# Kernel optimization log

Hardware: AMD Instinct MI355X
Metric: run time of the kernel (lower is better)

Reference implementation:

```python
import jax, jax.numpy as jnp
import numpy as np

NUM_SELECTS = 2
NOISE_EPS = 0.01
LOSS_COEF = 0.01
INV_SQRT2 = 0.7071067811865476


def _phi(z):
    # standard normal CDF
    return 0.5 * (1.0 + jax.lax.erf(z * INV_SQRT2))


def _cv_squared(v, eps=1e-10):
    # torch .var() uses unbiased estimator (ddof=1)
    return jnp.var(v, ddof=1) / (jnp.mean(v) ** 2 + eps)


def setup_inputs() -> dict:
    key = jax.random.key(0)
    ks = jax.random.split(key, 5)
    T, D, E = 8192, 4096, 16
    return {
        "x": jax.random.normal(ks[0], (T, D), jnp.float32),
        "gate_w1": jax.random.normal(ks[1], (E, D), jnp.float32) * 0.02,
        "gate_w2": jax.random.normal(ks[2], (E, E), jnp.float32) * 0.02,
        "noise_w": jax.random.normal(ks[3], (E, D), jnp.float32) * 0.02,
        "noise": jax.random.normal(ks[4], (T, E), jnp.float32),
    }


def reference(x, gate_w1, gate_w2, noise_w, noise):
    T = x.shape[0]
    # gate network: Linear -> tanh -> Linear (no biases)
    logits_gate = jnp.tanh(x @ gate_w1.T) @ gate_w2.T          # [T, E]
    noise_control = jax.nn.softplus(x @ noise_w.T) + NOISE_EPS  # [T, E]
    logits_noise = noise * noise_control                        # [T, E]
    logits = logits_gate + logits_noise

    # top (k+1) for load-balancing thresholds
    top_logits, top_indices = jax.lax.top_k(logits, NUM_SELECTS + 1)
    top_k_logits = top_logits[:, :NUM_SELECTS]
    top_k_indices = top_indices[:, :NUM_SELECTS]
    top_k_scores = jax.nn.softmax(top_k_logits, axis=1)

    # importance: scatter top-k scores back to [T, E]
    rows = jnp.arange(T)[:, None]
    scores_filtered = jnp.zeros_like(logits).at[rows, top_k_indices].set(top_k_scores)
    importance = scores_filtered.sum(0)  # [E]

    # load: prob each expert would be in the top-k under the noise model
    thr_in = top_logits[:, NUM_SELECTS][:, None]        # (k+1)-th largest
    thr_out = top_logits[:, NUM_SELECTS - 1][:, None]   # k-th largest
    is_in = logits_noise > thr_in
    prob_if_in = _phi((logits_gate - thr_in) / noise_control)
    prob_if_out = _phi((logits_gate - thr_out) / noise_control)
    load = jnp.where(is_in, prob_if_in, prob_if_out).sum(0)  # [E]

    gate_loss = (_cv_squared(importance) + _cv_squared(load)) * LOSS_COEF
    return top_k_indices, top_k_scores, gate_loss
```

## Files before the change

kernel.cpp:

```cpp
#include <hip/hip_runtime.h>
#include <math.h>

#define TT 8192
#define DD 4096

typedef float  f32x4  __attribute__((ext_vector_type(4)));
typedef short  bf16x8 __attribute__((ext_vector_type(8)));
typedef unsigned int u32;

__global__ __launch_bounds__(128)
void split_w(const float* __restrict__ gw1, const float* __restrict__ nw,
             u32* __restrict__ wfrag) {
  const int s = blockIdx.x;
  const int t = threadIdx.x;
  const int h = t >> 6, l = t & 63;
  const int e = h * 16 + (l & 15);
  const float* src = ((e < 16) ? (gw1 + (size_t)e * DD) : (nw + (size_t)(e - 16) * DD))
                     + s * 32 + ((l >> 4) << 3);
  float f[8];
  *(float4*)&f[0] = *(const float4*)src;
  *(float4*)&f[4] = *(const float4*)(src + 4);
  u32 u0[8], u1[8], u2[8];
#pragma unroll
  for (int i = 0; i < 8; ++i) {
    u0[i] = __float_as_uint(f[i]);
    const float r1 = f[i] - __uint_as_float(u0[i] & 0xFFFF0000u);
    u1[i] = __float_as_uint(r1);
    const float r2 = r1 - __uint_as_float(u1[i] & 0xFFFF0000u);
    u2[i] = __float_as_uint(r2);
  }
  const size_t base = ((size_t)s * 2 + h) * 256 + l * 4;
#define PK(U) make_uint4((U[0]>>16)|(U[1]&0xFFFF0000u), (U[2]>>16)|(U[3]&0xFFFF0000u), \
                         (U[4]>>16)|(U[5]&0xFFFF0000u), (U[6]>>16)|(U[7]&0xFFFF0000u))
  *(uint4*)(wfrag + base)                 = PK(u0);
  *(uint4*)(wfrag + base + 128 * 512)     = PK(u1);
  *(uint4*)(wfrag + base + 2 * 128 * 512) = PK(u2);
#undef PK
}

__global__ __launch_bounds__(512, 4)
void gate_mega(const float* __restrict__ x, const u32* __restrict__ wfrag,
               const float* __restrict__ noise, const float* __restrict__ gw2,
               float* __restrict__ out, float* __restrict__ part2) {
  __shared__ float red[8][1024];
  __shared__ float sg2[256];
  const int t = threadIdx.x;
  const int w = t >> 6, l = t & 63;
  const int bid = blockIdx.x;
  const int rt = (bid & 7) * 32 + (bid >> 3);
  if (t < 256) sg2[t] = gw2[t];

  const int r = l & 15, c = l >> 4;
  const float* xp0 = x + (size_t)(rt * 32 + r) * DD + w * 512 + (c << 3);
  const float* xp1 = xp0 + (size_t)16 * DD;
  const u32* wfl = wfrag + (size_t)l * 4 + (size_t)(w * 16) * 512;

  f32x4 g00 = {0,0,0,0}, g01 = g00, g02 = g00, n00 = g00, n01 = g00, n02 = g00;
  f32x4 g10 = g00, g11 = g00, g12 = g00, n10 = g00, n11 = g00, n12 = g00;

#define SPLIT8(FP, A0, A1, A2) \
  u32 pk_[12] __attribute__((aligned(16))); \
  { _Pragma("unroll") for (int p = 0; p < 4; ++p) { \
      const float fa = FP[2*p], fb = FP[2*p+1]; \
      const u32  a  = __float_as_uint(fa); \
      const float ra1 = fa - __uint_as_float(a & 0xFFFF0000u); \
      const u32  a1 = __float_as_uint(ra1); \
      const float ra2 = ra1 - __uint_as_float(a1 & 0xFFFF0000u); \
      const u32  a2 = __float_as_uint(ra2); \
      const u32  b  = __float_as_uint(fb); \
      const float rb1 = fb - __uint_as_float(b & 0xFFFF0000u); \
      const u32  b1 = __float_as_uint(rb1); \
      const float rb2 = rb1 - __uint_as_float(b1 & 0xFFFF0000u); \
      const u32  b2 = __float_as_uint(rb2); \
      pk_[p]     = (a  >> 16) | (b  & 0xFFFF0000u); \
      pk_[4 + p] = (a1 >> 16) | (b1 & 0xFFFF0000u); \
      pk_[8 + p] = (a2 >> 16) | (b2 & 0xFFFF0000u); } } \
  const bf16x8 A0 = *(const bf16x8*)&pk_[0]; \
  const bf16x8 A1 = *(const bf16x8*)&pk_[4]; \
  const bf16x8 A2 = *(const bf16x8*)&pk_[8];

#pragma unroll 2
  for (int sl = 0; sl < 16; ++sl) {
    const u32* wb = wfl + (size_t)sl * 512;
    const bf16x8 bg0 = *(const bf16x8*)(wb);
    const bf16x8 bn0 = *(const bf16x8*)(wb + 256);
    const bf16x8 bg1 = *(const bf16x8*)(wb + 128 * 512);
    const bf16x8 bn1 = *(const bf16x8*)(wb + 128 * 512 + 256);
    const bf16x8 bg2 = *(const bf16x8*)(wb + 2 * 128 * 512);
    const bf16x8 bn2 = *(const bf16x8*)(wb + 2 * 128 * 512 + 256);

    {
      float f[8];
      *(float4*)&f[0] = *(const float4*)(xp0 + sl * 32);
      *(float4*)&f[4] = *(const float4*)(xp0 + sl * 32 + 4);
      SPLIT8(f, a0, a1, a2)
      g00 = __builtin_amdgcn_mfma_f32_16x16x32_bf16(a0, bg0, g00, 0, 0, 0);
      n00 = __builtin_amdgcn_mfma_f32_16x16x32_bf16(a0, bn0, n00, 0, 0, 0);
      g01 = __builtin_amdgcn_mfma_f32_16x16x32_bf16(a0, bg1, g01, 0, 0, 0);
      n01 = __builtin_amdgcn_mfma_f32_16x16x32_bf16(a0, bn1, n01, 0, 0, 0);
      g02 = __builtin_amdgcn_mfma_f32_16x16x32_bf16(a1, bg0, g02, 0, 0, 0);
      n02 = __builtin_amdgcn_mfma_f32_16x16x32_bf16(a1, bn0, n02, 0, 0, 0);
      g00 = __builtin_amdgcn_mfma_f32_16x16x32_bf16(a0, bg2, g00, 0, 0, 0);
      n00 = __builtin_amdgcn_mfma_f32_16x16x32_bf16(a0, bn2, n00, 0, 0, 0);
      g01 = __builtin_amdgcn_mfma_f32_16x16x32_bf16(a1, bg1, g01, 0, 0, 0);
      n01 = __builtin_amdgcn_mfma_f32_16x16x32_bf16(a1, bn1, n01, 0, 0, 0);
      g02 = __builtin_amdgcn_mfma_f32_16x16x32_bf16(a2, bg0, g02, 0, 0, 0);
      n02 = __builtin_amdgcn_mfma_f32_16x16x32_bf16(a2, bn0, n02, 0, 0, 0);
    }
    {
      float f[8];
      *(float4*)&f[0] = *(const float4*)(xp1 + sl * 32);
      *(float4*)&f[4] = *(const float4*)(xp1 + sl * 32 + 4);
      SPLIT8(f, a0, a1, a2)
      g10 = __builtin_amdgcn_mfma_f32_16x16x32_bf16(a0, bg0, g10, 0, 0, 0);
      n10 = __builtin_amdgcn_mfma_f32_16x16x32_bf16(a0, bn0, n10, 0, 0, 0);
      g11 = __builtin_amdgcn_mfma_f32_16x16x32_bf16(a0, bg1, g11, 0, 0, 0);
      n11 = __builtin_amdgcn_mfma_f32_16x16x32_bf16(a0, bn1, n11, 0, 0, 0);
      g12 = __builtin_amdgcn_mfma_f32_16x16x32_bf16(a1, bg0, g12, 0, 0, 0);
      n12 = __builtin_amdgcn_mfma_f32_16x16x32_bf16(a1, bn0, n12, 0, 0, 0);
      g10 = __builtin_amdgcn_mfma_f32_16x16x32_bf16(a0, bg2, g10, 0, 0, 0);
      n10 = __builtin_amdgcn_mfma_f32_16x16x32_bf16(a0, bn2, n10, 0, 0, 0);
      g11 = __builtin_amdgcn_mfma_f32_16x16x32_bf16(a1, bg1, g11, 0, 0, 0);
      n11 = __builtin_amdgcn_mfma_f32_16x16x32_bf16(a1, bn1, n11, 0, 0, 0);
      g12 = __builtin_amdgcn_mfma_f32_16x16x32_bf16(a2, bg0, g12, 0, 0, 0);
      n12 = __builtin_amdgcn_mfma_f32_16x16x32_bf16(a2, bn0, n12, 0, 0, 0);
    }
  }
#undef SPLIT8

  const f32x4 cg0 = g00 + g01 + g02;
  const f32x4 cn0 = n00 + n01 + n02;
  const f32x4 cg1 = g10 + g11 + g12;
  const f32x4 cn1 = n10 + n11 + n12;
#pragma unroll
  for (int j = 0; j < 4; ++j) {
    red[w][r * 32 + (c * 4 + j)]             = cg0[j];
    red[w][(16 + r) * 32 + (c * 4 + j)]      = cn0[j];
    red[w][r * 32 + 16 + (c * 4 + j)]        = cg1[j];
    red[w][(16 + r) * 32 + 16 + (c * 4 + j)] = cn1[j];
  }
  __syncthreads();
#pragma unroll
  for (int idx = t; idx < 1024; idx += 512) {
    float s = red[0][idx];
#pragma unroll
    for (int ww = 1; ww < 8; ++ww) s += red[ww][idx];
    red[0][idx] = s;
  }
  __syncthreads();

  if (t < 32) {
    const int row = rt * 32 + t;
    float dot[32];
#pragma unroll
    for (int e = 0; e < 32; ++e) dot[e] = red[0][e * 32 + t];
    float h[16];
#pragma unroll
    for (int e = 0; e < 16; ++e) h[e] = tanhf(dot[e]);
    float lg[16], nc[16], ln[16], lo[16];
#pragma unroll
    for (int j = 0; j < 16; ++j) {
      float s = 0.f;
#pragma unroll
      for (int e = 0; e < 16; ++e) s = fmaf(h[e], sg2[j * 16 + e], s);
      lg[j] = s;
      const float v = dot[16 + j];
      nc[j] = fmaxf(v, 0.f) + log1pf(expf(-fabsf(v))) + 0.01f;
      ln[j] = noise[(size_t)row * 16 + j] * nc[j];
      lo[j] = lg[j] + ln[j];
    }
    int i0 = 0; float m0 = lo[0];
#pragma unroll
    for (int j = 1; j < 16; ++j) if (lo[j] > m0) { m0 = lo[j]; i0 = j; }
    int i1 = -1; float m1 = -1e30f;
#pragma unroll
    for (int j = 0; j < 16; ++j) if (j != i0 && lo[j] > m1) { m1 = lo[j]; i1 = j; }
    float m2 = -1e30f;
#pragma unroll
    for (int j = 0; j < 16; ++j) if (j != i0 && j != i1 && lo[j] > m2) m2 = lo[j];

    const float e1 = expf(m1 - m0);
    const float s0 = 1.f / (1.f + e1);
    const float s1 = e1 / (1.f + e1);
    out[(size_t)row * 2]             = (float)i0;
    out[(size_t)row * 2 + 1]         = (float)i1;
    out[16384 + (size_t)row * 2]     = s0;
    out[16384 + (size_t)row * 2 + 1] = s1;

    float cacc[32];
#pragma unroll
    for (int j = 0; j < 16; ++j) {
      cacc[j] = (j == i0) ? s0 : ((j == i1) ? s1 : 0.f);
      const bool in = ln[j] > m2;
      const float thr = in ? m2 : m1;
      const float z = (lg[j] - thr) / nc[j];
      cacc[16 + j] = 0.5f * (1.f + erff(z * 0.70710678118654752f));
    }
#pragma unroll
    for (int off = 1; off < 16; off <<= 1) {
#pragma unroll
      for (int k = 0; k < 32; ++k) cacc[k] += __shfl_xor(cacc[k], off, 16);
    }
    const int g = rt * 2 + (t >> 4);
    const int rr = t & 15;
    float v0 = 0.f, v1 = 0.f;
#pragma unroll
    for (int k = 0; k < 16; ++k) if (rr == k) { v0 = cacc[k]; v1 = cacc[16 + k]; }
    part2[(size_t)g * 32 + rr]      = v0;
    part2[(size_t)g * 32 + 16 + rr] = v1;
  }
}

__global__ __launch_bounds__(256)
void gate_loss_k(const float* __restrict__ part2, float* __restrict__ out) {
  __shared__ float sred[8][32];
  const int t = threadIdx.x;
  const int k = t & 31, s = t >> 5;
  float acc = 0.f;
#pragma unroll 8
  for (int i = 0; i < 64; ++i) acc += part2[(size_t)(s * 64 + i) * 32 + k];
  sred[s][k] = acc;
  __syncthreads();
  if (t == 0) {
    float res = 0.f;
    for (int g = 0; g < 2; ++g) {
      float vals[16];
      float mu = 0.f;
      for (int j = 0; j < 16; ++j) {
        float s2 = 0.f;
        for (int ss = 0; ss < 8; ++ss) s2 += sred[ss][g * 16 + j];
        vals[j] = s2;
        mu += s2;
      }
      mu *= (1.f / 16.f);
      float var = 0.f;
      for (int j = 0; j < 16; ++j) { const float d = vals[j] - mu; var += d * d; }
      var *= (1.f / 15.f);
      res += var / (mu * mu + 1e-10f);
    }
    out[32768] = res * 0.01f;
  }
}

extern "C" void kernel_launch(void* const* d_in, const int* in_sizes, int n_in,
                              void* d_out, int out_size, void* d_ws, size_t ws_size,
                              hipStream_t stream) {
  const float* x     = (const float*)d_in[0];
  const float* gw1   = (const float*)d_in[1];
  const float* gw2   = (const float*)d_in[2];
  const float* nw    = (const float*)d_in[3];
  const float* noise = (const float*)d_in[4];
  float* out   = (float*)d_out;
  u32*   wfrag = (u32*)d_ws;
  float* part2 = (float*)((char*)d_ws + (size_t)768 * 1024);
  split_w<<<128, 128, 0, stream>>>(gw1, nw, wfrag);
  gate_mega<<<256, 512, 0, stream>>>(x, wfrag, noise, gw2, out, part2);
  gate_loss_k<<<1, 256, 0, stream>>>(part2, out);
}
```

Baseline: 59.76 us.

## Fuse weight split, gate compute and loss into one cooperative kernel

Merges the three launches (weight bf16 split, main gate kernel, loss reduction) into a single cooperative kernel that uses grid-wide syncs between phases. This removes two kernel launch gaps and their inter-kernel dependencies. It also drops the row-tile swizzle in favour of rt = bid. The cost is two grid barriers, the need for all 256 blocks to be co-resident, and a final phase that runs on block 0 while every other block sits idle.

Result: slower. 108.4 us (+81.4%).

```diff
diff --git a/kernel.cpp b/kernel.cpp
--- a/kernel.cpp
+++ b/kernel.cpp
@@ -1,5 +1,8 @@
 #include <hip/hip_runtime.h>
+#include <hip/hip_cooperative_groups.h>
 #include <math.h>
+
+namespace cg = cooperative_groups;
 
 #define TT 8192
 #define DD 4096
@@ -8,46 +11,52 @@
 typedef short  bf16x8 __attribute__((ext_vector_type(8)));
 typedef unsigned int u32;
 
-__global__ __launch_bounds__(128)
-void split_w(const float* __restrict__ gw1, const float* __restrict__ nw,
-             u32* __restrict__ wfrag) {
-  const int s = blockIdx.x;
+__global__ __launch_bounds__(512, 4)
+void gate_fused(const float* __restrict__ x, u32* __restrict__ wfrag,
+                const float* __restrict__ noise, const float* __restrict__ gw2,
+                float* __restrict__ out, float* __restrict__ part2,
+                const float* __restrict__ gw1, const float* __restrict__ nw) {
+  cg::grid_group grid = cg::this_grid();
+  __shared__ float red[8][1024];
+  __shared__ float sg2[256];
+  __shared__ float sred[8][32];
   const int t = threadIdx.x;
-  const int h = t >> 6, l = t & 63;
-  const int e = h * 16 + (l & 15);
-  const float* src = ((e < 16) ? (gw1 + (size_t)e * DD) : (nw + (size_t)(e - 16) * DD))
-                     + s * 32 + ((l >> 4) << 3);
-  float f[8];
-  *(float4*)&f[0] = *(const float4*)src;
-  *(float4*)&f[4] = *(const float4*)(src + 4);
-  u32 u0[8], u1[8], u2[8];
-#pragma unroll
-  for (int i = 0; i < 8; ++i) {
-    u0[i] = __float_as_uint(f[i]);
-    const float r1 = f[i] - __uint_as_float(u0[i] & 0xFFFF0000u);
-    u1[i] = __float_as_uint(r1);
-    const float r2 = r1 - __uint_as_float(u1[i] & 0xFFFF0000u);
-    u2[i] = __float_as_uint(r2);
-  }
-  const size_t base = ((size_t)s * 2 + h) * 256 + l * 4;
+  const int bid = blockIdx.x;
+
+  {
+    const int tid = bid * 512 + t;
+    if (tid < 16384) {
+      const int s = tid >> 7;
+      const int tt = tid & 127;
+      const int h = tt >> 6, l = tt & 63;
+      const int e = h * 16 + (l & 15);
+      const float* src = ((e < 16) ? (gw1 + (size_t)e * DD) : (nw + (size_t)(e - 16) * DD))
+                         + s * 32 + ((l >> 4) << 3);
+      float f[8];
+      *(float4*)&f[0] = *(const float4*)src;
+      *(float4*)&f[4] = *(const float4*)(src + 4);
+      u32 u0[8], u1[8], u2[8];
+#pragma unroll
+      for (int i = 0; i < 8; ++i) {
+        u0[i] = __float_as_uint(f[i]);
+        const float r1 = f[i] - __uint_as_float(u0[i] & 0xFFFF0000u);
+        u1[i] = __float_as_uint(r1);
+        const float r2 = r1 - __uint_as_float(u1[i] & 0xFFFF0000u);
+        u2[i] = __float_as_uint(r2);
+      }
+      const size_t base = ((size_t)s * 2 + h) * 256 + l * 4;
 #define PK(U) make_uint4((U[0]>>16)|(U[1]&0xFFFF0000u), (U[2]>>16)|(U[3]&0xFFFF0000u), \
                          (U[4]>>16)|(U[5]&0xFFFF0000u), (U[6]>>16)|(U[7]&0xFFFF0000u))
-  *(uint4*)(wfrag + base)                 = PK(u0);
-  *(uint4*)(wfrag + base + 128 * 512)     = PK(u1);
-  *(uint4*)(wfrag + base + 2 * 128 * 512) = PK(u2);
+      *(uint4*)(wfrag + base)                 = PK(u0);
+      *(uint4*)(wfrag + base + 128 * 512)     = PK(u1);
+      *(uint4*)(wfrag + base + 2 * 128 * 512) = PK(u2);
 #undef PK
-}
-
-__global__ __launch_bounds__(512, 4)
-void gate_mega(const float* __restrict__ x, const u32* __restrict__ wfrag,
-               const float* __restrict__ noise, const float* __restrict__ gw2,
-               float* __restrict__ out, float* __restrict__ part2) {
-  __shared__ float red[8][1024];
-  __shared__ float sg2[256];
-  const int t = threadIdx.x;
+    }
+  }
+  grid.sync();
+
   const int w = t >> 6, l = t & 63;
-  const int bid = blockIdx.x;
-  const int rt = (bid & 7) * 32 + (bid >> 3);
+  const int rt = bid;
   if (t < 256) sg2[t] = gw2[t];
 
   const int r = l & 15, c = l >> 4;
@@ -209,36 +218,37 @@
     part2[(size_t)g * 32 + rr]      = v0;
     part2[(size_t)g * 32 + 16 + rr] = v1;
   }
-}
-
-__global__ __launch_bounds__(256)
-void gate_loss_k(const float* __restrict__ part2, float* __restrict__ out) {
-  __shared__ float sred[8][32];
-  const int t = threadIdx.x;
-  const int k = t & 31, s = t >> 5;
-  float acc = 0.f;
+
+  grid.sync();
+
+  if (bid == 0) {
+    if (t < 256) {
+      const int k = t & 31, s = t >> 5;
+      float acc = 0.f;
 #pragma unroll 8
-  for (int i = 0; i < 64; ++i) acc += part2[(size_t)(s * 64 + i) * 32 + k];
-  sred[s][k] = acc;
-  __syncthreads();
-  if (t == 0) {
-    float res = 0.f;
-    for (int g = 0; g < 2; ++g) {
-      float vals[16];
-      float mu = 0.f;
-      for (int j = 0; j < 16; ++j) {
-        float s2 = 0.f;
-        for (int ss = 0; ss < 8; ++ss) s2 += sred[ss][g * 16 + j];
-        vals[j] = s2;
-        mu += s2;
+      for (int i = 0; i < 64; ++i) acc += part2[(size_t)(s * 64 + i) * 32 + k];
+      sred[s][k] = acc;
+    }
+    __syncthreads();
+    if (t == 0) {
+      float res = 0.f;
+      for (int g = 0; g < 2; ++g) {
+        float vals[16];
+        float mu = 0.f;
+        for (int j = 0; j < 16; ++j) {
+          float s2 = 0.f;
+          for (int ss = 0; ss < 8; ++ss) s2 += sred[ss][g * 16 + j];
+          vals[j] = s2;
+          mu += s2;
+        }
+        mu *= (1.f / 16.f);
+        float var = 0.f;
+        for (int j = 0; j < 16; ++j) { const float d = vals[j] - mu; var += d * d; }
+        var *= (1.f / 15.f);
+        res += var / (mu * mu + 1e-10f);
       }
-      mu *= (1.f / 16.f);
-      float var = 0.f;
-      for (int j = 0; j < 16; ++j) { const float d = vals[j] - mu; var += d * d; }
-      var *= (1.f / 15.f);
-      res += var / (mu * mu + 1e-10f);
-    }
-    out[32768] = res * 0.01f;
+      out[32768] = res * 0.01f;
+    }
   }
 }
 
@@ -253,7 +263,9 @@
   float* out   = (float*)d_out;
   u32*   wfrag = (u32*)d_ws;
   float* part2 = (float*)((char*)d_ws + (size_t)768 * 1024);
-  split_w<<<128, 128, 0, stream>>>(gw1, nw, wfrag);
-  gate_mega<<<256, 512, 0, stream>>>(x, wfrag, noise, gw2, out, part2);
-  gate_loss_k<<<1, 256, 0, stream>>>(part2, out);
+
+  void* args[] = { (void*)&x, (void*)&wfrag, (void*)&noise, (void*)&gw2,
+                   (void*)&out, (void*)&part2, (void*)&gw1, (void*)&nw };
+  hipLaunchCooperativeKernel((const void*)gate_fused, dim3(256), dim3(512),
+                             args, 0, stream);
 }
```
